# Kernel tuning notes

Measured on AMD Instinct MI355X. Metric: run time of the kernel, lower is better.

Reference implementation:

```python
import jax, jax.numpy as jnp
import numpy as np

H = W = 192          # input spatial size
M = N = 96           # pooled grid (H//2, W//2)
NUM_NODES = M * N    # 9216
MAX_EDGES = 4 * NUM_NODES  # each node has at most 4 diagonal neighbors


def setup_inputs() -> dict:
    key = jax.random.key(0)
    k1, k2, k3 = jax.random.split(key, 3)
    d_coarse = jax.random.normal(k1, (1, H, W), dtype=jnp.float32)
    # torch.rand_like -> uniform [0,1); mean=0, stdev=1 in Noise module
    noise = jax.random.uniform(k2, (1, M, N), dtype=jnp.float32)
    # GraphDropout: `if self.train:` is always truthy -> dropout always applied
    dropout_mask = jax.random.bernoulli(k3, 0.5, (NUM_NODES, NUM_NODES))
    return {"d_coarse": d_coarse, "noise": noise,
            "dropout_mask": dropout_mask, "R_scale": 1}


def reference(d_coarse, noise, dropout_mask, R_scale):
    # MaxPool2d(kernel=2, stride=2) on [1, H, W]
    d_pool = d_coarse.reshape(1, M, 2, N, 2).max(axis=(2, 4))  # [1, M, N]
    # IntervalThreshold: computed on d_pool (pre-noise)
    threshold = (d_pool.max() - d_pool.min()) / min(M, N)
    # Noise: d_pool + uniform noise
    d = (d_pool + noise)[0]  # [M, N]

    # ReconGraph: `dx != 0 and dy != 0` -> ONLY diagonal neighbors.
    # labels[j, i] = count with i outer / j inner -> label(i, j) = i*N + j.
    lab = jnp.arange(NUM_NODES).reshape(M, N)
    adj = jnp.zeros((NUM_NODES, NUM_NODES), dtype=bool)
    # Two forward diagonal offsets cover all diagonal pairs; matrix is
    # symmetrized by setting both (l1, l2) and (l2, l1).
    pairs = [
        (lab[:-1, :-1], lab[1:, 1:], d[:-1, :-1], d[1:, 1:]),   # (dy,dx)=(1,1)
        (lab[:-1, 1:], lab[1:, :-1], d[:-1, 1:], d[1:, :-1]),   # (dy,dx)=(1,-1)
    ]
    for la, lb, a, b in pairs:
        conn = (jnp.abs(b - a) <= threshold).ravel()
        adj = adj.at[la.ravel(), lb.ravel()].set(conn)
        adj = adj.at[lb.ravel(), la.ravel()].set(conn)

    # GraphDropout (always active; mask is not symmetric)
    adj = adj & dropout_mask

    # convert_to_edge_index: COO indices of nonzeros, padded to static size
    rows, cols = jnp.nonzero(adj, size=MAX_EDGES, fill_value=NUM_NODES)
    return jnp.stack([rows, cols])  # [2, MAX_EDGES], sentinel = NUM_NODES
```

## Files before the change

### kernel.cpp

```cpp
#include <hip/hip_runtime.h>


#define HW 192
#define MM 96
#define NUM_NODES 9216
#define MAX_EDGES 36864
#define NT 1024
#define NPT 9

__global__ __launch_bounds__(NT) void extract_graph_kernel(
    const float* __restrict__ d_coarse,
    const float* __restrict__ noise,
    const int*   __restrict__ mask,
    int*         __restrict__ out)
{
    __shared__ float d_lds[NUM_NODES];
    __shared__ float redf[NT];
    __shared__ int   sc[NT];
    __shared__ float s_thr;

    const int t = threadIdx.x;

    float vmax = -3.0e38f, vmin = 3.0e38f;
    #pragma unroll
    for (int k = 0; k < NPT; ++k) {
        int l = k * NT + t;
        int i = l / MM;
        int j = l - i * MM;
        const float* r0 = d_coarse + (2 * i) * HW + 2 * j;
        float a = r0[0], b = r0[1], c = r0[HW], e = r0[HW + 1];
        float p = fmaxf(fmaxf(a, b), fmaxf(c, e));
        vmax = fmaxf(vmax, p);
        vmin = fminf(vmin, p);
        d_lds[l] = p + noise[l];
    }

    redf[t] = vmax;
    __syncthreads();
    for (int s = NT / 2; s > 0; s >>= 1) {
        if (t < s) redf[t] = fmaxf(redf[t], redf[t + s]);
        __syncthreads();
    }
    float gmax = redf[0];
    __syncthreads();
    redf[t] = vmin;
    __syncthreads();
    for (int s = NT / 2; s > 0; s >>= 1) {
        if (t < s) redf[t] = fminf(redf[t], redf[t + s]);
        __syncthreads();
    }
    if (t == 0) s_thr = (gmax - redf[0]) / 96.0f;
    __syncthreads();
    const float thr = s_thr;

    int flags[NPT];
    int cnt = 0;
    #pragma unroll
    for (int n = 0; n < NPT; ++n) {
        int l = t * NPT + n;
        int i = l / MM;
        int j = l - i * MM;
        float dl = d_lds[l];
        int f = 0;
        const size_t rowbase = (size_t)l * NUM_NODES;
        if (i > 0) {
            if (j > 0 && fabsf(d_lds[l - 97] - dl) <= thr &&
                mask[rowbase + (l - 97)] != 0) f |= 1;
            if (j < MM - 1 && fabsf(d_lds[l - 95] - dl) <= thr &&
                mask[rowbase + (l - 95)] != 0) f |= 2;
        }
        if (i < MM - 1) {
            if (j > 0 && fabsf(d_lds[l + 95] - dl) <= thr &&
                mask[rowbase + (l + 95)] != 0) f |= 4;
            if (j < MM - 1 && fabsf(d_lds[l + 97] - dl) <= thr &&
                mask[rowbase + (l + 97)] != 0) f |= 8;
        }
        flags[n] = f;
        cnt += __popc(f);
    }

    sc[t] = cnt;
    __syncthreads();
    for (int off = 1; off < NT; off <<= 1) {
        int v = sc[t] + ((t >= off) ? sc[t - off] : 0);
        __syncthreads();
        sc[t] = v;
        __syncthreads();
    }
    int pos = sc[t] - cnt;
    const int total = sc[NT - 1];

    #pragma unroll
    for (int n = 0; n < NPT; ++n) {
        int l = t * NPT + n;
        int f = flags[n];
        if (f & 1) { out[pos] = l; out[MAX_EDGES + pos] = l - 97; ++pos; }
        if (f & 2) { out[pos] = l; out[MAX_EDGES + pos] = l - 95; ++pos; }
        if (f & 4) { out[pos] = l; out[MAX_EDGES + pos] = l + 95; ++pos; }
        if (f & 8) { out[pos] = l; out[MAX_EDGES + pos] = l + 97; ++pos; }
    }

    for (int idx = total + t; idx < MAX_EDGES; idx += NT) {
        out[idx] = NUM_NODES;
        out[MAX_EDGES + idx] = NUM_NODES;
    }
}

extern "C" void kernel_launch(void* const* d_in, const int* in_sizes, int n_in,
                              void* d_out, int out_size, void* d_ws, size_t ws_size,
                              hipStream_t stream) {
    const float* d_coarse = (const float*)d_in[0];
    const float* noise    = (const float*)d_in[1];
    const int*   mask     = (const int*)d_in[2];
    int* out = (int*)d_out;

    extract_graph_kernel<<<1, NT, 0, stream>>>(d_coarse, noise, mask, out);
}
```

Before: 399.4 us.

## Split single-block graph kernel into three multi-block kernels with hierarchical scan

Replaces the single 1024-thread block with three kernels (pool+reduce, flag computation, compaction write), each using 36 blocks of 256 threads, with block-level partial results passed through workspace memory. Reductions and the prefix scan now use wavefront shuffles instead of LDS tree loops with many barriers. The aim is to spread the latency-bound scattered mask reads across many CUs instead of one. In exchange it adds two extra kernel launches and global-memory round trips for intermediates.

```diff
diff --git a/kernel.cpp b/kernel.cpp
--- a/kernel.cpp
+++ b/kernel.cpp
@@ -5,102 +5,129 @@
 #define MM 96
 #define NUM_NODES 9216
 #define MAX_EDGES 36864
-#define NT 1024
-#define NPT 9
+#define NB 36
+#define BT 256
 
-__global__ __launch_bounds__(NT) void extract_graph_kernel(
-    const float* __restrict__ d_coarse,
+
+__global__ __launch_bounds__(BT) void k_pool(
+    const float* __restrict__ dc,
     const float* __restrict__ noise,
+    float* __restrict__ d_buf,
+    float* __restrict__ blk_max,
+    float* __restrict__ blk_min)
+{
+    const int t = threadIdx.x;
+    const int l = blockIdx.x * BT + t;
+    const int i = l / MM, j = l - i * MM;
+    const float* r0 = dc + (2 * i) * HW + 2 * j;
+    float2 a = *(const float2*)r0;
+    float2 b = *(const float2*)(r0 + HW);
+    float p = fmaxf(fmaxf(a.x, a.y), fmaxf(b.x, b.y));
+    d_buf[l] = p + noise[l];
+
+    float mx = p, mn = p;
+    #pragma unroll
+    for (int off = 32; off > 0; off >>= 1) {
+        mx = fmaxf(mx, __shfl_down(mx, off, 64));
+        mn = fminf(mn, __shfl_down(mn, off, 64));
+    }
+    __shared__ float smx[4], smn[4];
+    const int lane = t & 63, wid = t >> 6;
+    if (lane == 0) { smx[wid] = mx; smn[wid] = mn; }
+    __syncthreads();
+    if (t == 0) {
+        blk_max[blockIdx.x] = fmaxf(fmaxf(smx[0], smx[1]), fmaxf(smx[2], smx[3]));
+        blk_min[blockIdx.x] = fminf(fminf(smn[0], smn[1]), fminf(smn[2], smn[3]));
+    }
+}
+
+__global__ __launch_bounds__(BT) void k_flags(
+    const float* __restrict__ d_buf,
+    const float* __restrict__ blk_max,
+    const float* __restrict__ blk_min,
     const int*   __restrict__ mask,
-    int*         __restrict__ out)
+    int* __restrict__ flags,
+    int* __restrict__ blk_cnt)
 {
-    __shared__ float d_lds[NUM_NODES];
-    __shared__ float redf[NT];
-    __shared__ int   sc[NT];
     __shared__ float s_thr;
-
     const int t = threadIdx.x;
-
-    float vmax = -3.0e38f, vmin = 3.0e38f;
-    #pragma unroll
-    for (int k = 0; k < NPT; ++k) {
-        int l = k * NT + t;
-        int i = l / MM;
-        int j = l - i * MM;
-        const float* r0 = d_coarse + (2 * i) * HW + 2 * j;
-        float a = r0[0], b = r0[1], c = r0[HW], e = r0[HW + 1];
-        float p = fmaxf(fmaxf(a, b), fmaxf(c, e));
-        vmax = fmaxf(vmax, p);
-        vmin = fminf(vmin, p);
-        d_lds[l] = p + noise[l];
+    if (t < 64) {
+        float mx = (t < NB) ? blk_max[t] : -3.0e38f;
+        float mn = (t < NB) ? blk_min[t] :  3.0e38f;
+        #pragma unroll
+        for (int off = 32; off > 0; off >>= 1) {
+            mx = fmaxf(mx, __shfl_down(mx, off, 64));
+            mn = fminf(mn, __shfl_down(mn, off, 64));
+        }
+        if (t == 0) s_thr = (mx - mn) / 96.0f;
     }
-
-    redf[t] = vmax;
-    __syncthreads();
-    for (int s = NT / 2; s > 0; s >>= 1) {
-        if (t < s) redf[t] = fmaxf(redf[t], redf[t + s]);
-        __syncthreads();
-    }
-    float gmax = redf[0];
-    __syncthreads();
-    redf[t] = vmin;
-    __syncthreads();
-    for (int s = NT / 2; s > 0; s >>= 1) {
-        if (t < s) redf[t] = fminf(redf[t], redf[t + s]);
-        __syncthreads();
-    }
-    if (t == 0) s_thr = (gmax - redf[0]) / 96.0f;
     __syncthreads();
     const float thr = s_thr;
 
-    int flags[NPT];
-    int cnt = 0;
+    const int l = blockIdx.x * BT + t;
+    const int i = l / MM, j = l - i * MM;
+    const float dl = d_buf[l];
+    const size_t rowbase = (size_t)l * NUM_NODES;
+    int f = 0;
+    if (i > 0) {
+        if (j > 0      && fabsf(d_buf[l - 97] - dl) <= thr && mask[rowbase + (l - 97)]) f |= 1;
+        if (j < MM - 1 && fabsf(d_buf[l - 95] - dl) <= thr && mask[rowbase + (l - 95)]) f |= 2;
+    }
+    if (i < MM - 1) {
+        if (j > 0      && fabsf(d_buf[l + 95] - dl) <= thr && mask[rowbase + (l + 95)]) f |= 4;
+        if (j < MM - 1 && fabsf(d_buf[l + 97] - dl) <= thr && mask[rowbase + (l + 97)]) f |= 8;
+    }
+    flags[l] = f;
+
+    int c = __popc(f);
     #pragma unroll
-    for (int n = 0; n < NPT; ++n) {
-        int l = t * NPT + n;
-        int i = l / MM;
-        int j = l - i * MM;
-        float dl = d_lds[l];
-        int f = 0;
-        const size_t rowbase = (size_t)l * NUM_NODES;
-        if (i > 0) {
-            if (j > 0 && fabsf(d_lds[l - 97] - dl) <= thr &&
-                mask[rowbase + (l - 97)] != 0) f |= 1;
-            if (j < MM - 1 && fabsf(d_lds[l - 95] - dl) <= thr &&
-                mask[rowbase + (l - 95)] != 0) f |= 2;
-        }
-        if (i < MM - 1) {
-            if (j > 0 && fabsf(d_lds[l + 95] - dl) <= thr &&
-                mask[rowbase + (l + 95)] != 0) f |= 4;
-            if (j < MM - 1 && fabsf(d_lds[l + 97] - dl) <= thr &&
-                mask[rowbase + (l + 97)] != 0) f |= 8;
-        }
-        flags[n] = f;
-        cnt += __popc(f);
+    for (int off = 32; off > 0; off >>= 1) c += __shfl_down(c, off, 64);
+    __shared__ int sc[4];
+    const int lane = t & 63, wid = t >> 6;
+    if (lane == 0) sc[wid] = c;
+    __syncthreads();
+    if (t == 0) blk_cnt[blockIdx.x] = sc[0] + sc[1] + sc[2] + sc[3];
+}
+
+__global__ __launch_bounds__(BT) void k_write(
+    const int* __restrict__ flags,
+    const int* __restrict__ blk_cnt,
+    int* __restrict__ out)
+{
+    const int t = threadIdx.x, b = blockIdx.x;
+
+    int blkoff = 0, total = 0;
+    #pragma unroll
+    for (int k = 0; k < NB; ++k) {
+        int c = blk_cnt[k];
+        if (k < b) blkoff += c;
+        total += c;
     }
 
-    sc[t] = cnt;
+    const int l = b * BT + t;
+    const int f = flags[l];
+    const int c = __popc(f);
+
+    int inc = c;
+    const int lane = t & 63, wid = t >> 6;
+    #pragma unroll
+    for (int off = 1; off < 64; off <<= 1) {
+        int v = __shfl_up(inc, off, 64);
+        if (lane >= off) inc += v;
+    }
+    __shared__ int wtot[4];
+    if (lane == 63) wtot[wid] = inc;
     __syncthreads();
-    for (int off = 1; off < NT; off <<= 1) {
-        int v = sc[t] + ((t >= off) ? sc[t - off] : 0);
-        __syncthreads();
-        sc[t] = v;
-        __syncthreads();
-    }
-    int pos = sc[t] - cnt;
-    const int total = sc[NT - 1];
+    int wpre = 0;
+    for (int k = 0; k < wid; ++k) wpre += wtot[k];
 
-    #pragma unroll
-    for (int n = 0; n < NPT; ++n) {
-        int l = t * NPT + n;
-        int f = flags[n];
-        if (f & 1) { out[pos] = l; out[MAX_EDGES + pos] = l - 97; ++pos; }
-        if (f & 2) { out[pos] = l; out[MAX_EDGES + pos] = l - 95; ++pos; }
-        if (f & 4) { out[pos] = l; out[MAX_EDGES + pos] = l + 95; ++pos; }
-        if (f & 8) { out[pos] = l; out[MAX_EDGES + pos] = l + 97; ++pos; }
-    }
+    int pos = blkoff + wpre + (inc - c);
+    if (f & 1) { out[pos] = l; out[MAX_EDGES + pos] = l - 97; ++pos; }
+    if (f & 2) { out[pos] = l; out[MAX_EDGES + pos] = l - 95; ++pos; }
+    if (f & 4) { out[pos] = l; out[MAX_EDGES + pos] = l + 95; ++pos; }
+    if (f & 8) { out[pos] = l; out[MAX_EDGES + pos] = l + 97; ++pos; }
 
-    for (int idx = total + t; idx < MAX_EDGES; idx += NT) {
+    for (int idx = total + b * BT + t; idx < MAX_EDGES; idx += NUM_NODES) {
         out[idx] = NUM_NODES;
         out[MAX_EDGES + idx] = NUM_NODES;
     }
@@ -114,5 +141,14 @@
     const int*   mask     = (const int*)d_in[2];
     int* out = (int*)d_out;
 
-    extract_graph_kernel<<<1, NT, 0, stream>>>(d_coarse, noise, mask, out);
+    float* ws      = (float*)d_ws;
+    float* d_buf   = ws;
+    float* blk_max = ws + 9216;
+    float* blk_min = ws + 9252;
+    int*   flags   = (int*)(ws + 9288);
+    int*   blk_cnt = (int*)(ws + 18504);
+
+    k_pool <<<NB, BT, 0, stream>>>(d_coarse, noise, d_buf, blk_max, blk_min);
+    k_flags<<<NB, BT, 0, stream>>>(d_buf, blk_max, blk_min, mask, flags, blk_cnt);
+    k_write<<<NB, BT, 0, stream>>>(flags, blk_cnt, out);
 }
```

New measurement: 376.2 us. 5.8% less time.

## Split edge extraction across nine blocks with decoupled lookback prefix scan

Applied to the files above, without the earlier changes.

Moves from one 1024-thread block to nine blocks, one node per thread, so the scattered dropout-mask reads are spread over more compute units. Block offsets into the output come from a lookback over per-block totals published in the workspace with a valid bit. The LDS tree reductions and scan become wavefront shuffle reductions and scans, and the pooled-input loads use float2. Each block still recomputes the full pooling and threshold, and the workspace flags are never cleared, so a later call, or garbage in a fresh workspace, can hand a block stale offsets.

```diff
diff --git a/kernel.cpp b/kernel.cpp
--- a/kernel.cpp
+++ b/kernel.cpp
@@ -5,104 +5,122 @@
 #define MM 96
 #define NUM_NODES 9216
 #define MAX_EDGES 36864
-#define NT 1024
-#define NPT 9
+#define NBLK 9
+#define BT 1024
+#define VALID_BIT 0x40000000
 
-__global__ __launch_bounds__(NT) void extract_graph_kernel(
-    const float* __restrict__ d_coarse,
+__global__ __launch_bounds__(BT) void extract_graph(
+    const float* __restrict__ dc,
     const float* __restrict__ noise,
     const int*   __restrict__ mask,
-    int*         __restrict__ out)
+    int*         __restrict__ out,
+    int*         __restrict__ blk_state)
 {
     __shared__ float d_lds[NUM_NODES];
-    __shared__ float redf[NT];
-    __shared__ int   sc[NT];
+    __shared__ float smx[16], smn[16];
+    __shared__ int   wsum[16];
     __shared__ float s_thr;
+    __shared__ int   s_blkoff, s_btot;
 
     const int t = threadIdx.x;
+    const int b = blockIdx.x;
+    const int lane = t & 63, wid = t >> 6;
 
     float vmax = -3.0e38f, vmin = 3.0e38f;
     #pragma unroll
-    for (int k = 0; k < NPT; ++k) {
-        int l = k * NT + t;
-        int i = l / MM;
-        int j = l - i * MM;
-        const float* r0 = d_coarse + (2 * i) * HW + 2 * j;
-        float a = r0[0], b = r0[1], c = r0[HW], e = r0[HW + 1];
-        float p = fmaxf(fmaxf(a, b), fmaxf(c, e));
+    for (int k = 0; k < NUM_NODES / BT; ++k) {
+        int l = k * BT + t;
+        int i = l / MM, j = l - i * MM;
+        const float* r0 = dc + (2 * i) * HW + 2 * j;
+        float2 a = *(const float2*)r0;
+        float2 c = *(const float2*)(r0 + HW);
+        float p = fmaxf(fmaxf(a.x, a.y), fmaxf(c.x, c.y));
         vmax = fmaxf(vmax, p);
         vmin = fminf(vmin, p);
         d_lds[l] = p + noise[l];
     }
-
-    redf[t] = vmax;
+    #pragma unroll
+    for (int off = 32; off > 0; off >>= 1) {
+        vmax = fmaxf(vmax, __shfl_down(vmax, off, 64));
+        vmin = fminf(vmin, __shfl_down(vmin, off, 64));
+    }
+    if (lane == 0) { smx[wid] = vmax; smn[wid] = vmin; }
     __syncthreads();
-    for (int s = NT / 2; s > 0; s >>= 1) {
-        if (t < s) redf[t] = fmaxf(redf[t], redf[t + s]);
-        __syncthreads();
+    if (t == 0) {
+        float mx = smx[0], mn = smn[0];
+        #pragma unroll
+        for (int k = 1; k < 16; ++k) {
+            mx = fmaxf(mx, smx[k]);
+            mn = fminf(mn, smn[k]);
+        }
+        s_thr = (mx - mn) / 96.0f;
     }
-    float gmax = redf[0];
-    __syncthreads();
-    redf[t] = vmin;
-    __syncthreads();
-    for (int s = NT / 2; s > 0; s >>= 1) {
-        if (t < s) redf[t] = fminf(redf[t], redf[t + s]);
-        __syncthreads();
-    }
-    if (t == 0) s_thr = (gmax - redf[0]) / 96.0f;
     __syncthreads();
     const float thr = s_thr;
 
-    int flags[NPT];
-    int cnt = 0;
+    const int l = b * BT + t;
+    const int i = l / MM, j = l - i * MM;
+    const float dl = d_lds[l];
+    const size_t rowbase = (size_t)l * NUM_NODES;
+    int f = 0;
+    if (i > 0) {
+        if (j > 0      && fabsf(d_lds[l - 97] - dl) <= thr && mask[rowbase + (l - 97)]) f |= 1;
+        if (j < MM - 1 && fabsf(d_lds[l - 95] - dl) <= thr && mask[rowbase + (l - 95)]) f |= 2;
+    }
+    if (i < MM - 1) {
+        if (j > 0      && fabsf(d_lds[l + 95] - dl) <= thr && mask[rowbase + (l + 95)]) f |= 4;
+        if (j < MM - 1 && fabsf(d_lds[l + 97] - dl) <= thr && mask[rowbase + (l + 97)]) f |= 8;
+    }
+    const int cnt = __popc(f);
+
+    int inc = cnt;
     #pragma unroll
-    for (int n = 0; n < NPT; ++n) {
-        int l = t * NPT + n;
-        int i = l / MM;
-        int j = l - i * MM;
-        float dl = d_lds[l];
-        int f = 0;
-        const size_t rowbase = (size_t)l * NUM_NODES;
-        if (i > 0) {
-            if (j > 0 && fabsf(d_lds[l - 97] - dl) <= thr &&
-                mask[rowbase + (l - 97)] != 0) f |= 1;
-            if (j < MM - 1 && fabsf(d_lds[l - 95] - dl) <= thr &&
-                mask[rowbase + (l - 95)] != 0) f |= 2;
+    for (int off = 1; off < 64; off <<= 1) {
+        int v = __shfl_up(inc, off, 64);
+        if (lane >= off) inc += v;
+    }
+    if (lane == 63) wsum[wid] = inc;
+    __syncthreads();
+    int wpre = 0;
+    for (int k = 0; k < wid; ++k) wpre += wsum[k];
+    const int local_excl = wpre + inc - cnt;
+
+    if (wid == 0) {
+        if (lane == 0) {
+            int btot = 0;
+            #pragma unroll
+            for (int k = 0; k < 16; ++k) btot += wsum[k];
+            s_btot = btot;
+            __hip_atomic_store(&blk_state[b], VALID_BIT | btot,
+                               __ATOMIC_RELEASE, __HIP_MEMORY_SCOPE_AGENT);
         }
-        if (i < MM - 1) {
-            if (j > 0 && fabsf(d_lds[l + 95] - dl) <= thr &&
-                mask[rowbase + (l + 95)] != 0) f |= 4;
-            if (j < MM - 1 && fabsf(d_lds[l + 97] - dl) <= thr &&
-                mask[rowbase + (l + 97)] != 0) f |= 8;
+        int v = 0;
+        if (lane < b) {
+            int s;
+            do {
+                s = __hip_atomic_load(&blk_state[lane],
+                                      __ATOMIC_ACQUIRE, __HIP_MEMORY_SCOPE_AGENT);
+            } while (!(s & VALID_BIT));
+            v = s & 0xFFFF;
         }
-        flags[n] = f;
-        cnt += __popc(f);
+        #pragma unroll
+        for (int off = 32; off > 0; off >>= 1) v += __shfl_down(v, off, 64);
+        if (lane == 0) s_blkoff = v;
     }
+    __syncthreads();
 
-    sc[t] = cnt;
-    __syncthreads();
-    for (int off = 1; off < NT; off <<= 1) {
-        int v = sc[t] + ((t >= off) ? sc[t - off] : 0);
-        __syncthreads();
-        sc[t] = v;
-        __syncthreads();
-    }
-    int pos = sc[t] - cnt;
-    const int total = sc[NT - 1];
+    int pos = s_blkoff + local_excl;
+    if (f & 1) { out[pos] = l; out[MAX_EDGES + pos] = l - 97; ++pos; }
+    if (f & 2) { out[pos] = l; out[MAX_EDGES + pos] = l - 95; ++pos; }
+    if (f & 4) { out[pos] = l; out[MAX_EDGES + pos] = l + 95; ++pos; }
+    if (f & 8) { out[pos] = l; out[MAX_EDGES + pos] = l + 97; ++pos; }
 
-    #pragma unroll
-    for (int n = 0; n < NPT; ++n) {
-        int l = t * NPT + n;
-        int f = flags[n];
-        if (f & 1) { out[pos] = l; out[MAX_EDGES + pos] = l - 97; ++pos; }
-        if (f & 2) { out[pos] = l; out[MAX_EDGES + pos] = l - 95; ++pos; }
-        if (f & 4) { out[pos] = l; out[MAX_EDGES + pos] = l + 95; ++pos; }
-        if (f & 8) { out[pos] = l; out[MAX_EDGES + pos] = l + 97; ++pos; }
-    }
-
-    for (int idx = total + t; idx < MAX_EDGES; idx += NT) {
-        out[idx] = NUM_NODES;
-        out[MAX_EDGES + idx] = NUM_NODES;
+    if (b == NBLK - 1) {
+        const int total = s_blkoff + s_btot;
+        for (int idx = total + t; idx < MAX_EDGES; idx += BT) {
+            out[idx] = NUM_NODES;
+            out[MAX_EDGES + idx] = NUM_NODES;
+        }
     }
 }
 
@@ -112,7 +130,8 @@
     const float* d_coarse = (const float*)d_in[0];
     const float* noise    = (const float*)d_in[1];
     const int*   mask     = (const int*)d_in[2];
-    int* out = (int*)d_out;
+    int* out       = (int*)d_out;
+    int* blk_state = (int*)d_ws;
 
-    extract_graph_kernel<<<1, NT, 0, stream>>>(d_coarse, noise, mask, out);
+    extract_graph<<<NBLK, BT, 0, stream>>>(d_coarse, noise, mask, out, blk_state);
 }
```

Result: faster. 377.8 us (-5.4%).
